# Kernel tuning notes

Measured on AMD Instinct MI355X. Metric: run time of the kernel, lower is better.

## Reference

```python
import jax, jax.numpy as jnp
import numpy as np

S, B, H = 4096, 64, 256
D = 2.0
SIGMA = D / 2.0


def setup_inputs() -> dict:
    key = jax.random.key(0)
    ks = jax.random.split(key, 7)
    return {
        "e": jax.random.normal(ks[0], (S, B, H), dtype=jnp.float32),
        "d": jax.random.normal(ks[1], (1, B, H), dtype=jnp.float32),
        "W_a": jax.random.normal(ks[2], (H, H), dtype=jnp.float32) / np.sqrt(H),
        "W_p": jax.random.normal(ks[3], (H, H), dtype=jnp.float32) / np.sqrt(H),
        "v_p": jax.random.normal(ks[4], (H, 1), dtype=jnp.float32) / np.sqrt(H),
        "lin_w": jax.random.normal(ks[5], (H, 2 * H), dtype=jnp.float32) / np.sqrt(2 * H),
        "lin_b": jax.random.normal(ks[6], (H,), dtype=jnp.float32) * 0.01,
    }


def reference(e, d, W_a, W_p, v_p, lin_w, lin_b):
    s = e.shape[0]
    # alignment: scores over source positions, softmax along S (dim 0 in torch)
    scores = jnp.sum((d @ W_a) * e, axis=2)          # [S, B]
    a = jax.nn.softmax(scores, axis=0)               # [S, B]
    # predictive position gating (Luong local-p attention)
    h = jnp.tanh(d[0] @ W_p)                         # [B, H]
    p_center = jax.nn.sigmoid((h @ v_p)[:, 0])[None, :] * s   # [1, B]
    pos = jnp.arange(s, dtype=e.dtype)[:, None]      # [S, 1]
    diff = p_center - pos                            # [S, B]
    mask = (jnp.abs(diff) <= D).astype(e.dtype)
    p = jnp.exp(-(diff * diff) / (2.0 * SIGMA * SIGMA)) * mask  # [S, B]
    w = a * p                                        # [S, B]
    context = jnp.einsum('sbh,sb->bh', e, w)[None]   # [1, B, H]
    x = jnp.concatenate([context, d], axis=2)        # [1, B, 2H]
    out = jax.nn.relu(x @ lin_w.T + lin_b)           # dropout = identity (eval)
    return out, w
```

## Files before the change

### kernel.cpp

```cpp
#include <hip/hip_runtime.h>
#include <math.h>

constexpr int S_ = 4096;
constexpr int B_ = 64;
constexpr int H_ = 256;


__global__ __launch_bounds__(256) void k1_prep(const float* __restrict__ d,
                                               const float* __restrict__ W_a,
                                               const float* __restrict__ W_p,
                                               const float* __restrict__ v_p,
                                               float* __restrict__ dW,
                                               float* __restrict__ pc) {
  int b = blockIdx.x;
  int h = threadIdx.x;
  float acc_a = 0.f, acc_p = 0.f;
  const float* db = d + b * H_;
  for (int k = 0; k < H_; ++k) {
    float dv = db[k];
    acc_a = fmaf(dv, W_a[k * H_ + h], acc_a);
    acc_p = fmaf(dv, W_p[k * H_ + h], acc_p);
  }
  dW[b * H_ + h] = acc_a;
  float prod = tanhf(acc_p) * v_p[h];
  __shared__ float red[256];
  red[h] = prod;
  __syncthreads();
  for (int st = 128; st > 0; st >>= 1) {
    if (h < st) red[h] += red[h + st];
    __syncthreads();
  }
  if (h == 0) {
    pc[b] = (float)S_ / (1.f + expf(-red[0]));
  }
}

__global__ __launch_bounds__(256) void k2_scores(const float* __restrict__ e,
                                                 const float* __restrict__ dW,
                                                 float* __restrict__ scores) {
  int t = threadIdx.x;
  int wave = t >> 6;
  int lane = t & 63;
  int bl = lane >> 2;
  int sub = lane & 3;
  int b = wave * 16 + bl;
  int s0 = blockIdx.x * 4;

  const float4* dW4 = (const float4*)(dW + b * H_);
  float4 wreg[16];
#pragma unroll
  for (int j = 0; j < 16; ++j) wreg[j] = dW4[sub + 4 * j];

  float sc[4];
#pragma unroll
  for (int r = 0; r < 4; ++r) {
    const float4* erow = (const float4*)(e + ((size_t)(s0 + r) * B_ + b) * H_);
    float acc = 0.f;
#pragma unroll
    for (int half = 0; half < 2; ++half) {
      float4 ev[8];
#pragma unroll
      for (int j = 0; j < 8; ++j) ev[j] = erow[sub + 4 * (half * 8 + j)];
#pragma unroll
      for (int j = 0; j < 8; ++j) {
        const float4 wv = wreg[half * 8 + j];
        acc = fmaf(ev[j].x, wv.x, fmaf(ev[j].y, wv.y,
              fmaf(ev[j].z, wv.z, fmaf(ev[j].w, wv.w, acc))));
      }
    }
    acc += __shfl_xor(acc, 1, 64);
    acc += __shfl_xor(acc, 2, 64);
    sc[r] = acc;
  }

  __shared__ float tile[4][64];
  if (sub == 0) {
#pragma unroll
    for (int r = 0; r < 4; ++r) tile[r][b] = sc[r];
  }
  __syncthreads();
  int b_out = t >> 2, r = t & 3;
  scores[b_out * S_ + s0 + r] = tile[r][b_out];
}

__global__ __launch_bounds__(256) void kF(const float* __restrict__ scores,
                                          const float* __restrict__ pc,
                                          const float* __restrict__ e,
                                          const float* __restrict__ d,
                                          const float* __restrict__ lin_w,
                                          const float* __restrict__ lin_b,
                                          float* __restrict__ out,
                                          float* __restrict__ w_out) {
  int b = blockIdx.x;
  int t = threadIdx.x;
  const float* sc = scores + b * S_;
  float v[16];
  float lm = -INFINITY;
#pragma unroll
  for (int k = 0; k < 16; ++k) {
    v[k] = sc[t + k * 256];
    lm = fmaxf(lm, v[k]);
  }
  __shared__ float red[256];
  red[t] = lm;
  __syncthreads();
  for (int st = 128; st > 0; st >>= 1) {
    if (t < st) red[t] = fmaxf(red[t], red[t + st]);
    __syncthreads();
  }
  float mb = red[0];
  __syncthreads();
  float ls = 0.f;
#pragma unroll
  for (int k = 0; k < 16; ++k) ls += expf(v[k] - mb);
  red[t] = ls;
  __syncthreads();
  for (int st = 128; st > 0; st >>= 1) {
    if (t < st) red[t] += red[t + st];
    __syncthreads();
  }
  float inv_l = 1.f / red[0];
  float pcb = pc[b];
#pragma unroll
  for (int k = 0; k < 16; ++k) {
    int s = t + k * 256;
    float diff = pcb - (float)s;
    float p = (fabsf(diff) <= 2.f) ? expf(-0.5f * diff * diff) : 0.f;
    w_out[(size_t)s * B_ + b] = expf(v[k] - mb) * inv_l * p;
  }
  int s0 = max(0, (int)ceilf(pcb - 2.f));
  int s1 = min(S_ - 1, (int)floorf(pcb + 2.f));
  float ctx = 0.f;
  for (int s = s0; s <= s1; ++s) {
    float diff = pcb - (float)s;
    float wv = expf(sc[s] - mb) * inv_l * expf(-0.5f * diff * diff);
    ctx = fmaf(wv, e[((size_t)s * B_ + b) * H_ + t], ctx);
  }
  __shared__ float x[512];
  x[t] = ctx;
  x[256 + t] = d[b * H_ + t];
  __syncthreads();
  float acc = lin_b[t];
  const float4* lw = (const float4*)(lin_w + t * 2 * H_);
  const float4* xv = (const float4*)x;
#pragma unroll 4
  for (int k = 0; k < 128; ++k) {
    float4 a4 = lw[k];
    float4 b4 = xv[k];
    acc += a4.x * b4.x + a4.y * b4.y + a4.z * b4.z + a4.w * b4.w;
  }
  out[b * H_ + t] = fmaxf(acc, 0.f);
}

extern "C" void kernel_launch(void* const* d_in, const int* in_sizes, int n_in,
                              void* d_out, int out_size, void* d_ws, size_t ws_size,
                              hipStream_t stream) {
  const float* e     = (const float*)d_in[0];
  const float* d     = (const float*)d_in[1];
  const float* W_a   = (const float*)d_in[2];
  const float* W_p   = (const float*)d_in[3];
  const float* v_p   = (const float*)d_in[4];
  const float* lin_w = (const float*)d_in[5];
  const float* lin_b = (const float*)d_in[6];

  float* out   = (float*)d_out;
  float* w_out = out + B_ * H_;

  float* ws     = (float*)d_ws;
  float* dW     = ws;
  float* pc     = ws + 16384;
  float* scores = ws + 16448;

  k1_prep<<<B_, 256, 0, stream>>>(d, W_a, W_p, v_p, dW, pc);
  k2_scores<<<S_ / 4, 256, 0, stream>>>(e, dW, scores);
  kF<<<B_, 256, 0, stream>>>(scores, pc, e, d, lin_w, lin_b, out, w_out);
}
```

Measured before the change: 86.05 us.

## Fuse scores, softmax and context into one kernel with last-block finalize

Merges the score kernel and the softmax/context kernel into one launch. Each block emits partial max/sum-exp statistics and stashes window scores, and the last 64 blocks to arrive, ordered by an atomic counter, spin-wait and then do the per-batch finalize. The dense w output is now zeroed by a memset, with only the window entries written, which drops the full scores round-trip and the 64-block softmax pass. The prep kernel splits its K loop across 1024 threads. The spin-wait assumes all blocks become resident or finish, and it adds a memset of w_out.

```diff
diff --git a/kernel.cpp b/kernel.cpp
--- a/kernel.cpp
+++ b/kernel.cpp
@@ -4,159 +4,191 @@
 constexpr int S_ = 4096;
 constexpr int B_ = 64;
 constexpr int H_ = 256;
-
-
-__global__ __launch_bounds__(256) void k1_prep(const float* __restrict__ d,
-                                               const float* __restrict__ W_a,
-                                               const float* __restrict__ W_p,
-                                               const float* __restrict__ v_p,
-                                               float* __restrict__ dW,
-                                               float* __restrict__ pc) {
-  int b = blockIdx.x;
-  int h = threadIdx.x;
-  float acc_a = 0.f, acc_p = 0.f;
+constexpr int NBLK_B = 1024;
+
+
+__global__ __launch_bounds__(1024) void kA_prep(const float* __restrict__ d,
+                                                const float* __restrict__ W_a,
+                                                const float* __restrict__ W_p,
+                                                const float* __restrict__ v_p,
+                                                float* __restrict__ dW,
+                                                float* __restrict__ pc) {
+  const int b = blockIdx.x;
+  const int t = threadIdx.x;
+  const int h = t & 255;
+  const int kc = t >> 8;
   const float* db = d + b * H_;
-  for (int k = 0; k < H_; ++k) {
+  float aa = 0.f, ap = 0.f;
+#pragma unroll 8
+  for (int k = kc * 64; k < kc * 64 + 64; ++k) {
     float dv = db[k];
-    acc_a = fmaf(dv, W_a[k * H_ + h], acc_a);
-    acc_p = fmaf(dv, W_p[k * H_ + h], acc_p);
-  }
-  dW[b * H_ + h] = acc_a;
-  float prod = tanhf(acc_p) * v_p[h];
-  __shared__ float red[256];
-  red[h] = prod;
+    aa = fmaf(dv, W_a[k * H_ + h], aa);
+    ap = fmaf(dv, W_p[k * H_ + h], ap);
+  }
+  __shared__ float redA[1024];
+  __shared__ float redB[1024];
+  redA[t] = aa;
+  redB[t] = ap;
+  __syncthreads();
+  if (t < 256) {
+    float dwa = redA[t] + redA[t + 256] + redA[t + 512] + redA[t + 768];
+    float dwp = redB[t] + redB[t + 256] + redB[t + 512] + redB[t + 768];
+    dW[b * H_ + t] = dwa;
+    redA[t] = tanhf(dwp) * v_p[t];
+  }
   __syncthreads();
   for (int st = 128; st > 0; st >>= 1) {
-    if (h < st) red[h] += red[h + st];
+    if (t < st) redA[t] += redA[t + st];
     __syncthreads();
   }
-  if (h == 0) {
-    pc[b] = (float)S_ / (1.f + expf(-red[0]));
-  }
+  if (t == 0) pc[b] = (float)S_ / (1.f + expf(-redA[0]));
 }
 
-__global__ __launch_bounds__(256) void k2_scores(const float* __restrict__ e,
-                                                 const float* __restrict__ dW,
-                                                 float* __restrict__ scores) {
-  int t = threadIdx.x;
-  int wave = t >> 6;
-  int lane = t & 63;
-  int bl = lane >> 2;
-  int sub = lane & 3;
-  int b = wave * 16 + bl;
-  int s0 = blockIdx.x * 4;
-
-  const float4* dW4 = (const float4*)(dW + b * H_);
-  float4 wreg[16];
-#pragma unroll
-  for (int j = 0; j < 16; ++j) wreg[j] = dW4[sub + 4 * j];
-
-  float sc[4];
-#pragma unroll
-  for (int r = 0; r < 4; ++r) {
-    const float4* erow = (const float4*)(e + ((size_t)(s0 + r) * B_ + b) * H_);
-    float acc = 0.f;
-#pragma unroll
-    for (int half = 0; half < 2; ++half) {
-      float4 ev[8];
-#pragma unroll
-      for (int j = 0; j < 8; ++j) ev[j] = erow[sub + 4 * (half * 8 + j)];
-#pragma unroll
-      for (int j = 0; j < 8; ++j) {
-        const float4 wv = wreg[half * 8 + j];
-        acc = fmaf(ev[j].x, wv.x, fmaf(ev[j].y, wv.y,
-              fmaf(ev[j].z, wv.z, fmaf(ev[j].w, wv.w, acc))));
+__global__ __launch_bounds__(256) void kB_main(const float* __restrict__ e,
+                                               const float* __restrict__ dW,
+                                               const float* __restrict__ pc,
+                                               const float* __restrict__ d,
+                                               const float* __restrict__ lin_w,
+                                               const float* __restrict__ lin_b,
+                                               float* __restrict__ swin,
+                                               float* __restrict__ mpart,
+                                               float* __restrict__ lpart,
+                                               unsigned int* __restrict__ counter,
+                                               float* __restrict__ out,
+                                               float* __restrict__ w_out) {
+  const int t = threadIdx.x;
+  const int blk = blockIdx.x;
+  __shared__ float tile[4][64];
+  __shared__ unsigned int ordS;
+
+  {
+    const int wave = t >> 6, lane = t & 63;
+    const int bl = lane >> 2, sub = lane & 3;
+    const int b = wave * 16 + bl;
+    const int s0 = blk * 4;
+    const float4* dW4 = (const float4*)(dW + b * H_);
+    float4 wreg[16];
+#pragma unroll
+    for (int j = 0; j < 16; ++j) wreg[j] = dW4[sub + 4 * j];
+#pragma unroll
+    for (int r = 0; r < 4; ++r) {
+      const float4* erow = (const float4*)(e + ((size_t)(s0 + r) * B_ + b) * H_);
+      float acc = 0.f;
+#pragma unroll
+      for (int half = 0; half < 2; ++half) {
+        float4 ev[8];
+#pragma unroll
+        for (int j = 0; j < 8; ++j) ev[j] = erow[sub + 4 * (half * 8 + j)];
+#pragma unroll
+        for (int j = 0; j < 8; ++j) {
+          const float4 wv = wreg[half * 8 + j];
+          acc = fmaf(ev[j].x, wv.x, fmaf(ev[j].y, wv.y,
+                fmaf(ev[j].z, wv.z, fmaf(ev[j].w, wv.w, acc))));
+        }
       }
+      acc += __shfl_xor(acc, 1, 64);
+      acc += __shfl_xor(acc, 2, 64);
+      if (sub == 0) tile[r][b] = acc;
     }
-    acc += __shfl_xor(acc, 1, 64);
-    acc += __shfl_xor(acc, 2, 64);
-    sc[r] = acc;
-  }
-
-  __shared__ float tile[4][64];
-  if (sub == 0) {
-#pragma unroll
-    for (int r = 0; r < 4; ++r) tile[r][b] = sc[r];
-  }
-  __syncthreads();
-  int b_out = t >> 2, r = t & 3;
-  scores[b_out * S_ + s0 + r] = tile[r][b_out];
-}
-
-__global__ __launch_bounds__(256) void kF(const float* __restrict__ scores,
-                                          const float* __restrict__ pc,
-                                          const float* __restrict__ e,
-                                          const float* __restrict__ d,
-                                          const float* __restrict__ lin_w,
-                                          const float* __restrict__ lin_b,
-                                          float* __restrict__ out,
-                                          float* __restrict__ w_out) {
-  int b = blockIdx.x;
-  int t = threadIdx.x;
-  const float* sc = scores + b * S_;
-  float v[16];
-  float lm = -INFINITY;
-#pragma unroll
-  for (int k = 0; k < 16; ++k) {
-    v[k] = sc[t + k * 256];
-    lm = fmaxf(lm, v[k]);
-  }
-  __shared__ float red[256];
-  red[t] = lm;
+  }
+  __syncthreads();
+  if (t < 64) {
+    const int b = t;
+    const int sbase = blk * 4;
+    float m0 = fmaxf(fmaxf(tile[0][b], tile[1][b]), fmaxf(tile[2][b], tile[3][b]));
+    float ls = expf(tile[0][b] - m0) + expf(tile[1][b] - m0) +
+               expf(tile[2][b] - m0) + expf(tile[3][b] - m0);
+    mpart[blk * B_ + b] = m0;
+    lpart[blk * B_ + b] = ls;
+    const float pcb = pc[b];
+#pragma unroll
+    for (int r = 0; r < 4; ++r) {
+      int s = sbase + r;
+      if (fabsf(pcb - (float)s) <= 2.f) swin[b * 8 + (s & 7)] = tile[r][b];
+    }
+  }
+  __syncthreads();
+  if (t == 0) {
+    __threadfence();
+    ordS = atomicAdd(counter, 1u);
+  }
+  __syncthreads();
+  const unsigned int ord = ordS;
+  if (ord < NBLK_B - B_) return;
+  const int bf = (int)ord - (NBLK_B - B_);
+
+  if (t == 0) {
+    while (__hip_atomic_load(counter, __ATOMIC_ACQUIRE, __HIP_MEMORY_SCOPE_AGENT) < (unsigned)NBLK_B)
+      __builtin_amdgcn_s_sleep(8);
+  }
+  __syncthreads();
+  __threadfence();
+
+  float* red = &tile[0][0];
+  float rm[4], rl[4];
+#pragma unroll
+  for (int j = 0; j < 4; ++j) {
+    int i = t + j * 256;
+    rm[j] = mpart[i * B_ + bf];
+    rl[j] = lpart[i * B_ + bf];
+  }
+  float mloc = fmaxf(fmaxf(rm[0], rm[1]), fmaxf(rm[2], rm[3]));
+  red[t] = mloc;
   __syncthreads();
   for (int st = 128; st > 0; st >>= 1) {
     if (t < st) red[t] = fmaxf(red[t], red[t + st]);
     __syncthreads();
   }
-  float mb = red[0];
-  __syncthreads();
-  float ls = 0.f;
-#pragma unroll
-  for (int k = 0; k < 16; ++k) ls += expf(v[k] - mb);
-  red[t] = ls;
+  const float M = red[0];
+  __syncthreads();
+  float lsum = rl[0] * expf(rm[0] - M) + rl[1] * expf(rm[1] - M) +
+               rl[2] * expf(rm[2] - M) + rl[3] * expf(rm[3] - M);
+  red[t] = lsum;
   __syncthreads();
   for (int st = 128; st > 0; st >>= 1) {
     if (t < st) red[t] += red[t + st];
     __syncthreads();
   }
-  float inv_l = 1.f / red[0];
-  float pcb = pc[b];
-#pragma unroll
-  for (int k = 0; k < 16; ++k) {
-    int s = t + k * 256;
+  const float L = red[0];
+  __syncthreads();
+
+  __shared__ float wsh[8];
+  __shared__ float xbuf[512];
+  const float pcb = pc[bf];
+  const int s0 = max(0, (int)ceilf(pcb - 2.f));
+  const int s1 = min(S_ - 1, (int)floorf(pcb + 2.f));
+  const int nw = s1 - s0 + 1;
+  if (t < nw) {
+    int s = s0 + t;
     float diff = pcb - (float)s;
-    float p = (fabsf(diff) <= 2.f) ? expf(-0.5f * diff * diff) : 0.f;
-    w_out[(size_t)s * B_ + b] = expf(v[k] - mb) * inv_l * p;
-  }
-  int s0 = max(0, (int)ceilf(pcb - 2.f));
-  int s1 = min(S_ - 1, (int)floorf(pcb + 2.f));
+    float w = expf(swin[bf * 8 + (s & 7)] - M) / L * expf(-0.5f * diff * diff);
+    w_out[(size_t)s * B_ + bf] = w;
+    wsh[t] = w;
+  }
+  __syncthreads();
   float ctx = 0.f;
-  for (int s = s0; s <= s1; ++s) {
-    float diff = pcb - (float)s;
-    float wv = expf(sc[s] - mb) * inv_l * expf(-0.5f * diff * diff);
-    ctx = fmaf(wv, e[((size_t)s * B_ + b) * H_ + t], ctx);
-  }
-  __shared__ float x[512];
-  x[t] = ctx;
-  x[256 + t] = d[b * H_ + t];
+  for (int j = 0; j < nw; ++j)
+    ctx = fmaf(wsh[j], e[((size_t)(s0 + j) * B_ + bf) * H_ + t], ctx);
+  xbuf[t] = ctx;
+  xbuf[256 + t] = d[bf * H_ + t];
   __syncthreads();
   float acc = lin_b[t];
   const float4* lw = (const float4*)(lin_w + t * 2 * H_);
-  const float4* xv = (const float4*)x;
-#pragma unroll 4
+  const float4* xv = (const float4*)xbuf;
+#pragma unroll 8
   for (int k = 0; k < 128; ++k) {
     float4 a4 = lw[k];
     float4 b4 = xv[k];
     acc += a4.x * b4.x + a4.y * b4.y + a4.z * b4.z + a4.w * b4.w;
   }
-  out[b * H_ + t] = fmaxf(acc, 0.f);
+  out[bf * H_ + t] = fmaxf(acc, 0.f);
 }
 
 extern "C" void kernel_launch(void* const* d_in, const int* in_sizes, int n_in,
                               void* d_out, int out_size, void* d_ws, size_t ws_size,
                               hipStream_t stream) {
   const float* e     = (const float*)d_in[0];
-  const float* d     = (const float*)d_in[1];
+  const float* dd    = (const float*)d_in[1];
   const float* W_a   = (const float*)d_in[2];
   const float* W_p   = (const float*)d_in[3];
   const float* v_p   = (const float*)d_in[4];
@@ -169,9 +201,14 @@
   float* ws     = (float*)d_ws;
   float* dW     = ws;
   float* pc     = ws + 16384;
-  float* scores = ws + 16448;
-
-  k1_prep<<<B_, 256, 0, stream>>>(d, W_a, W_p, v_p, dW, pc);
-  k2_scores<<<S_ / 4, 256, 0, stream>>>(e, dW, scores);
-  kF<<<B_, 256, 0, stream>>>(scores, pc, e, d, lin_w, lin_b, out, w_out);
+  unsigned int* counter = (unsigned int*)(ws + 16448);
+  float* swin   = ws + 16512;
+  float* mpart  = ws + 17024;
+  float* lpart  = ws + 82560;
+
+  hipMemsetAsync(counter, 0, sizeof(unsigned int), stream);
+  hipMemsetAsync(w_out, 0, (size_t)S_ * B_ * sizeof(float), stream);
+  kA_prep<<<B_, 1024, 0, stream>>>(dd, W_a, W_p, v_p, dW, pc);
+  kB_main<<<NBLK_B, 256, 0, stream>>>(e, dW, pc, dd, lin_w, lin_b,
+                                      swin, mpart, lpart, counter, out, w_out);
 }
```

After: 137.2 us. 1.59x slower.
